# Kernel tuning notes

Hardware: AMD Instinct MI355X
Metric: run time of the kernel (lower is better)

## Reference

```python
import jax, jax.numpy as jnp
import numpy as np
from math import sqrt

D_MODEL = 512
HEADS = 8
D_K = D_MODEL // HEADS
DIM_FFN = 2048
EPS = 1e-6


def setup_inputs() -> dict:
    key = jax.random.key(0)
    ks = jax.random.split(key, 16)
    b, s = 2, 256
    inp = {
        "x": jax.random.normal(ks[0], (b, s, D_MODEL), dtype=jnp.float32),
        "connection_bias_k": jax.random.normal(ks[1], (b, s, s, D_MODEL), dtype=jnp.float32) * 0.02,
        "connection_bias_v": jax.random.normal(ks[2], (b, s, s, D_MODEL), dtype=jnp.float32) * 0.02,
        "mask": jnp.zeros((b, s), dtype=jnp.int32),
        "Wq": jax.random.normal(ks[3], (D_MODEL, D_MODEL), dtype=jnp.float32) / sqrt(D_MODEL),
        "bq": jnp.zeros((D_MODEL,), dtype=jnp.float32),
        "Wk": jax.random.normal(ks[4], (D_MODEL, D_MODEL), dtype=jnp.float32) / sqrt(D_MODEL),
        "bk": jnp.zeros((D_MODEL,), dtype=jnp.float32),
        "Wv": jax.random.normal(ks[5], (D_MODEL, D_MODEL), dtype=jnp.float32) / sqrt(D_MODEL),
        "bv": jnp.zeros((D_MODEL,), dtype=jnp.float32),
        "Wo": jax.random.normal(ks[6], (D_MODEL, D_MODEL), dtype=jnp.float32) / sqrt(D_MODEL),
        "bo": jnp.zeros((D_MODEL,), dtype=jnp.float32),
        "alpha1": jnp.ones((D_MODEL,), dtype=jnp.float32),
        "beta1": jnp.zeros((D_MODEL,), dtype=jnp.float32),
        "alpha2": jnp.ones((D_MODEL,), dtype=jnp.float32),
        "beta2": jnp.zeros((D_MODEL,), dtype=jnp.float32),
        "W1": jax.random.normal(ks[7], (DIM_FFN, D_MODEL), dtype=jnp.float32) / sqrt(D_MODEL),
        "b1": jnp.zeros((DIM_FFN,), dtype=jnp.float32),
        "W2": jax.random.normal(ks[8], (D_MODEL, DIM_FFN), dtype=jnp.float32) / sqrt(DIM_FFN),
        "b2": jnp.zeros((D_MODEL,), dtype=jnp.float32),
    }
    return inp


def _norm(x, alpha, beta):
    # torch .std() is unbiased (ddof=1); note std is added to eps OUTSIDE variance
    mu = jnp.mean(x, axis=-1, keepdims=True)
    sd = jnp.std(x, axis=-1, ddof=1, keepdims=True)
    return alpha * (x - mu) / (sd + EPS) + beta


def reference(x, connection_bias_k, connection_bias_v, mask,
              Wq, bq, Wk, bk, Wv, bv, Wo, bo,
              alpha1, beta1, alpha2, beta2, W1, b1, W2, b2):
    b, s, _ = x.shape
    h, dk = HEADS, D_K

    x2 = _norm(x, alpha1, beta1)
    # projections -> [b, h, s, dk]
    q = (x2 @ Wq.T + bq).reshape(b, s, h, dk).transpose(0, 2, 1, 3)
    k = (x2 @ Wk.T + bk).reshape(b, s, h, dk).transpose(0, 2, 1, 3)
    v = (x2 @ Wv.T + bv).reshape(b, s, h, dk).transpose(0, 2, 1, 3)

    # biases reshaped to (b, s1, s2, h, dk); biased_k[b,h,i,j] = k[b,h,j] + bias[b,j,i,h]
    bk_r = connection_bias_k.reshape(b, s, s, h, dk)
    bv_r = connection_bias_v.reshape(b, s, s, h, dk)

    # scores[b,h,i,j] = q_i . (k_j + bias_k[b,j,i,h]) / sqrt(dk)
    scores = (jnp.einsum('bhid,bhjd->bhij', q, k)
              + jnp.einsum('bhid,bjihd->bhij', q, bk_r)) / sqrt(dk)

    # mask [b,s] -> [b,1,s,1], broadcast over heads and key dim (matches torch)
    m = mask[:, None, :, None]
    scores = jnp.where(m == 1, -1e9, scores)
    attn = jax.nn.softmax(scores, axis=-1)

    # out[b,h,i,d] = sum_j attn[b,h,i,j] * (v[b,h,j] + bias_v[b,j,i,h])
    out = (jnp.einsum('bhij,bhjd->bhid', attn, v)
           + jnp.einsum('bhij,bjihd->bhid', attn, bv_r))
    concat = out.transpose(0, 2, 1, 3).reshape(b, s, D_MODEL)
    attn_out = concat @ Wo.T + bo

    x = x + attn_out
    x2 = _norm(x, alpha2, beta2)
    ff = jax.nn.relu(x2 @ W1.T + b1) @ W2.T + b2
    return x + ff
```

## Files before the change

### kernel.cpp

```cpp
#include <hip/hip_runtime.h>
#include <math.h>

#define D_MODEL 512
#define NHEADS 8
#define DK 64
#define DFFN 2048

__global__ __launch_bounds__(256) void ln_kernel(
    const float* __restrict__ x, const float* __restrict__ alpha,
    const float* __restrict__ beta, float* __restrict__ y) {
  int row = blockIdx.x;
  int t = threadIdx.x;
  const float* xr = x + (size_t)row * D_MODEL;
  float2 v = ((const float2*)xr)[t];
  __shared__ float rs[256], rq[256];
  rs[t] = v.x + v.y;
  rq[t] = v.x * v.x + v.y * v.y;
  __syncthreads();
  for (int o = 128; o > 0; o >>= 1) {
    if (t < o) { rs[t] += rs[t + o]; rq[t] += rq[t + o]; }
    __syncthreads();
  }
  float mu = rs[0] * (1.0f / D_MODEL);
  float var = (rq[0] - (float)D_MODEL * mu * mu) * (1.0f / (D_MODEL - 1));
  float inv = 1.0f / (sqrtf(fmaxf(var, 0.0f)) + 1e-6f);
  float2 a2 = ((const float2*)alpha)[t];
  float2 b2 = ((const float2*)beta)[t];
  float2 o2;
  o2.x = a2.x * (v.x - mu) * inv + b2.x;
  o2.y = a2.y * (v.y - mu) * inv + b2.y;
  ((float2*)(y + (size_t)row * D_MODEL))[t] = o2;
}

template <int RELU>
__global__ __launch_bounds__(256) void gemm_nt(
    const float* __restrict__ A, const float* __restrict__ B,
    const float* __restrict__ bias, const float* __restrict__ res,
    float* __restrict__ C, int M, int N, int K) {
  __shared__ float As[16][65];
  __shared__ float Bs[16][65];
  int t = threadIdx.x;
  int tx = t & 15, ty = t >> 4;
  int ldRow = t >> 2;
  int ldCol = (t & 3) << 2;
  const float* Ap = A + (size_t)(blockIdx.y * 64 + ldRow) * K + ldCol;
  const float* Bp = B + (size_t)(blockIdx.x * 64 + ldRow) * K + ldCol;
  float acc[4][4] = {};
  for (int k0 = 0; k0 < K; k0 += 16) {
    float4 a4 = *(const float4*)(Ap + k0);
    float4 b4 = *(const float4*)(Bp + k0);
    As[ldCol + 0][ldRow] = a4.x; As[ldCol + 1][ldRow] = a4.y;
    As[ldCol + 2][ldRow] = a4.z; As[ldCol + 3][ldRow] = a4.w;
    Bs[ldCol + 0][ldRow] = b4.x; Bs[ldCol + 1][ldRow] = b4.y;
    Bs[ldCol + 2][ldRow] = b4.z; Bs[ldCol + 3][ldRow] = b4.w;
    __syncthreads();
#pragma unroll
    for (int kk = 0; kk < 16; ++kk) {
      float a[4], b[4];
#pragma unroll
      for (int i = 0; i < 4; ++i) a[i] = As[kk][ty * 4 + i];
#pragma unroll
      for (int j = 0; j < 4; ++j) b[j] = Bs[kk][tx * 4 + j];
#pragma unroll
      for (int i = 0; i < 4; ++i)
#pragma unroll
        for (int j = 0; j < 4; ++j) acc[i][j] += a[i] * b[j];
    }
    __syncthreads();
  }
  int row0 = blockIdx.y * 64 + ty * 4;
  int col0 = blockIdx.x * 64 + tx * 4;
#pragma unroll
  for (int i = 0; i < 4; ++i) {
#pragma unroll
    for (int j = 0; j < 4; ++j) {
      float v = acc[i][j] + bias[col0 + j];
      if (res) v += res[(size_t)(row0 + i) * N + col0 + j];
      if (RELU) v = fmaxf(v, 0.0f);
      C[(size_t)(row0 + i) * N + col0 + j] = v;
    }
  }
}

struct Triple { const float* B; const float* bias; float* C; };
struct Triple3 { Triple t[3]; };

__global__ __launch_bounds__(256) void gemm_qkv(
    const float* __restrict__ A, Triple3 p3, int M, int N, int K) {
  Triple tr = p3.t[blockIdx.z];
  const float* __restrict__ B = tr.B;
  __shared__ float As[16][65];
  __shared__ float Bs[16][65];
  int t = threadIdx.x;
  int tx = t & 15, ty = t >> 4;
  int ldRow = t >> 2;
  int ldCol = (t & 3) << 2;
  const float* Ap = A + (size_t)(blockIdx.y * 64 + ldRow) * K + ldCol;
  const float* Bp = B + (size_t)(blockIdx.x * 64 + ldRow) * K + ldCol;
  float acc[4][4] = {};
  for (int k0 = 0; k0 < K; k0 += 16) {
    float4 a4 = *(const float4*)(Ap + k0);
    float4 b4 = *(const float4*)(Bp + k0);
    As[ldCol + 0][ldRow] = a4.x; As[ldCol + 1][ldRow] = a4.y;
    As[ldCol + 2][ldRow] = a4.z; As[ldCol + 3][ldRow] = a4.w;
    Bs[ldCol + 0][ldRow] = b4.x; Bs[ldCol + 1][ldRow] = b4.y;
    Bs[ldCol + 2][ldRow] = b4.z; Bs[ldCol + 3][ldRow] = b4.w;
    __syncthreads();
#pragma unroll
    for (int kk = 0; kk < 16; ++kk) {
      float a[4], b[4];
#pragma unroll
      for (int i = 0; i < 4; ++i) a[i] = As[kk][ty * 4 + i];
#pragma unroll
      for (int j = 0; j < 4; ++j) b[j] = Bs[kk][tx * 4 + j];
#pragma unroll
      for (int i = 0; i < 4; ++i)
#pragma unroll
        for (int j = 0; j < 4; ++j) acc[i][j] += a[i] * b[j];
    }
    __syncthreads();
  }
  int row0 = blockIdx.y * 64 + ty * 4;
  int col0 = blockIdx.x * 64 + tx * 4;
#pragma unroll
  for (int i = 0; i < 4; ++i) {
#pragma unroll
    for (int j = 0; j < 4; ++j) {
      tr.C[(size_t)(row0 + i) * N + col0 + j] = acc[i][j] + tr.bias[col0 + j];
    }
  }
}

__global__ __launch_bounds__(256) void gemm_nt_splitk(
    const float* __restrict__ A, const float* __restrict__ B,
    float* __restrict__ P, int M, int N, int K, int KC) {
  __shared__ float As[16][65];
  __shared__ float Bs[16][65];
  int t = threadIdx.x;
  int tx = t & 15, ty = t >> 4;
  int ldRow = t >> 2;
  int ldCol = (t & 3) << 2;
  int kbase = blockIdx.z * KC;
  const float* Ap = A + (size_t)(blockIdx.y * 64 + ldRow) * K + ldCol + kbase;
  const float* Bp = B + (size_t)(blockIdx.x * 64 + ldRow) * K + ldCol + kbase;
  float acc[4][4] = {};
  for (int k0 = 0; k0 < KC; k0 += 16) {
    float4 a4 = *(const float4*)(Ap + k0);
    float4 b4 = *(const float4*)(Bp + k0);
    As[ldCol + 0][ldRow] = a4.x; As[ldCol + 1][ldRow] = a4.y;
    As[ldCol + 2][ldRow] = a4.z; As[ldCol + 3][ldRow] = a4.w;
    Bs[ldCol + 0][ldRow] = b4.x; Bs[ldCol + 1][ldRow] = b4.y;
    Bs[ldCol + 2][ldRow] = b4.z; Bs[ldCol + 3][ldRow] = b4.w;
    __syncthreads();
#pragma unroll
    for (int kk = 0; kk < 16; ++kk) {
      float a[4], b[4];
#pragma unroll
      for (int i = 0; i < 4; ++i) a[i] = As[kk][ty * 4 + i];
#pragma unroll
      for (int j = 0; j < 4; ++j) b[j] = Bs[kk][tx * 4 + j];
#pragma unroll
      for (int i = 0; i < 4; ++i)
#pragma unroll
        for (int j = 0; j < 4; ++j) acc[i][j] += a[i] * b[j];
    }
    __syncthreads();
  }
  int row0 = blockIdx.y * 64 + ty * 4;
  int col0 = blockIdx.x * 64 + tx * 4;
  float* Pz = P + (size_t)blockIdx.z * M * N;
#pragma unroll
  for (int i = 0; i < 4; ++i)
#pragma unroll
    for (int j = 0; j < 4; ++j)
      Pz[(size_t)(row0 + i) * N + col0 + j] = acc[i][j];
}

__global__ __launch_bounds__(256) void splitk_reduce(
    const float* __restrict__ P, const float* __restrict__ bias,
    const float* __restrict__ res, float* __restrict__ C,
    int MN, int N, int Z) {
  int idx = blockIdx.x * 256 + threadIdx.x;
  if (idx >= MN) return;
  float v = bias[idx % N] + res[idx];
  for (int z = 0; z < Z; ++z) v += P[(size_t)z * MN + idx];
  C[idx] = v;
}

__global__ __launch_bounds__(256) void attn_kernel(
    const float* __restrict__ q, const float* __restrict__ k,
    const float* __restrict__ v, const float* __restrict__ cbk,
    const float* __restrict__ cbv, const int* __restrict__ mask,
    float* __restrict__ concat, int s) {
  int i = blockIdx.x % s;
  int h = (blockIdx.x / s) % NHEADS;
  int b = blockIdx.x / (s * NHEADS);
  int t = threadIdx.x;

  __shared__ __align__(16) float qs[DK];
  __shared__ float p[256];
  __shared__ float red[256];
  __shared__ float outp[4][DK];

  size_t qbase = ((size_t)(b * s + i)) * D_MODEL + h * DK;
  if (t < DK) qs[t] = q[qbase + t];
  __syncthreads();

  int lane16 = t & 15;
  int jg = t >> 4;
  float4 q4 = ((const float4*)qs)[lane16];
  for (int jt = 0; jt < s; jt += 16) {
    int j = jt + jg;
    size_t kb = ((size_t)(b * s + j)) * D_MODEL + h * DK + lane16 * 4;
    float4 k4 = *(const float4*)(k + kb);
    size_t bb = (((size_t)(b * s + j)) * s + i) * D_MODEL + h * DK + lane16 * 4;
    float4 b4 = *(const float4*)(cbk + bb);
    float part = q4.x * (k4.x + b4.x) + q4.y * (k4.y + b4.y) +
                 q4.z * (k4.z + b4.z) + q4.w * (k4.w + b4.w);
    part += __shfl_xor(part, 1);
    part += __shfl_xor(part, 2);
    part += __shfl_xor(part, 4);
    part += __shfl_xor(part, 8);
    if (lane16 == 0) p[j] = part * 0.125f;
  }
  __syncthreads();

  float sc = p[t];
  if (mask[b * s + i] == 1) sc = -1e9f;
  red[t] = sc;
  __syncthreads();
  for (int o = 128; o > 0; o >>= 1) {
    if (t < o) red[t] = fmaxf(red[t], red[t + o]);
    __syncthreads();
  }
  float mx = red[0];
  __syncthreads();
  float e = expf(sc - mx);
  p[t] = e;
  red[t] = e;
  __syncthreads();
  for (int o = 128; o > 0; o >>= 1) {
    if (t < o) red[t] += red[t + o];
    __syncthreads();
  }
  float inv = 1.0f / red[0];

  int d = t & 63;
  int c = t >> 6;
  float acc = 0.0f;
  int chunk = s >> 2;
  for (int jj = 0; jj < chunk; ++jj) {
    int j = c * chunk + jj;
    size_t vb = ((size_t)(b * s + j)) * D_MODEL + h * DK + d;
    size_t bb = (((size_t)(b * s + j)) * s + i) * D_MODEL + h * DK + d;
    acc += p[j] * (v[vb] + cbv[bb]);
  }
  outp[c][d] = acc;
  __syncthreads();
  if (t < DK) {
    float o = (outp[0][t] + outp[1][t] + outp[2][t] + outp[3][t]) * inv;
    concat[((size_t)(b * s + i)) * D_MODEL + h * DK + t] = o;
  }
}

extern "C" void kernel_launch(void* const* d_in, const int* in_sizes, int n_in,
                              void* d_out, int out_size, void* d_ws, size_t ws_size,
                              hipStream_t stream) {
  const float* x      = (const float*)d_in[0];
  const float* cbk    = (const float*)d_in[1];
  const float* cbv    = (const float*)d_in[2];
  const int*   mask   = (const int*)d_in[3];
  const float* Wq     = (const float*)d_in[4];
  const float* bq     = (const float*)d_in[5];
  const float* Wk     = (const float*)d_in[6];
  const float* bk     = (const float*)d_in[7];
  const float* Wv     = (const float*)d_in[8];
  const float* bv     = (const float*)d_in[9];
  const float* Wo     = (const float*)d_in[10];
  const float* bo     = (const float*)d_in[11];
  const float* alpha1 = (const float*)d_in[12];
  const float* beta1  = (const float*)d_in[13];
  const float* alpha2 = (const float*)d_in[14];
  const float* beta2  = (const float*)d_in[15];
  const float* W1     = (const float*)d_in[16];
  const float* b1     = (const float*)d_in[17];
  const float* W2     = (const float*)d_in[18];
  const float* b2     = (const float*)d_in[19];

  int bs = in_sizes[0] / D_MODEL;
  int s  = in_sizes[1] / in_sizes[0];
  int b  = bs / s;

  float* ws = (float*)d_ws;
  float* x2      = ws;
  float* qb      = x2 + (size_t)bs * D_MODEL;
  float* kb      = qb + (size_t)bs * D_MODEL;
  float* vb      = kb + (size_t)bs * D_MODEL;
  float* concat  = vb + (size_t)bs * D_MODEL;
  float* xres    = concat + (size_t)bs * D_MODEL;
  float* x2b     = xres + (size_t)bs * D_MODEL;
  float* f1      = x2b + (size_t)bs * D_MODEL;
  float* partial = f1 + (size_t)bs * DFFN;

  ln_kernel<<<bs, 256, 0, stream>>>(x, alpha1, beta1, x2);

  Triple3 p3;
  p3.t[0] = {Wq, bq, qb};
  p3.t[1] = {Wk, bk, kb};
  p3.t[2] = {Wv, bv, vb};
  gemm_qkv<<<dim3(D_MODEL / 64, bs / 64, 3), 256, 0, stream>>>(x2, p3, bs, D_MODEL, D_MODEL);

  attn_kernel<<<b * NHEADS * s, 256, 0, stream>>>(qb, kb, vb, cbk, cbv, mask, concat, s);

  gemm_nt<0><<<dim3(D_MODEL / 64, bs / 64), 256, 0, stream>>>(
      concat, Wo, bo, x, xres, bs, D_MODEL, D_MODEL);

  ln_kernel<<<bs, 256, 0, stream>>>(xres, alpha2, beta2, x2b);

  gemm_nt<1><<<dim3(DFFN / 64, bs / 64), 256, 0, stream>>>(
      x2b, W1, b1, nullptr, f1, bs, DFFN, D_MODEL);

  gemm_nt_splitk<<<dim3(D_MODEL / 64, bs / 64, 4), 256, 0, stream>>>(
      f1, W2, partial, bs, D_MODEL, DFFN, DFFN / 4);
  splitk_reduce<<<(bs * D_MODEL + 255) / 256, 256, 0, stream>>>(
      partial, b2, xres, (float*)d_out, bs * D_MODEL, D_MODEL, 4);
}
```

Baseline: 727.8 us.

## Switch GEMMs to bf16 MFMA and restructure attention per token across heads

```diff
diff --git a/kernel.cpp b/kernel.cpp
--- a/kernel.cpp
+++ b/kernel.cpp
@@ -6,9 +6,12 @@
 #define DK 64
 #define DFFN 2048
 
+typedef __attribute__((ext_vector_type(8))) __bf16 bf16x8;
+typedef __attribute__((ext_vector_type(4))) float floatx4;
+
 __global__ __launch_bounds__(256) void ln_kernel(
     const float* __restrict__ x, const float* __restrict__ alpha,
-    const float* __restrict__ beta, float* __restrict__ y) {
+    const float* __restrict__ beta, __bf16* __restrict__ y) {
   int row = blockIdx.x;
   int t = threadIdx.x;
   const float* xr = x + (size_t)row * D_MODEL;
@@ -26,241 +29,178 @@
   float inv = 1.0f / (sqrtf(fmaxf(var, 0.0f)) + 1e-6f);
   float2 a2 = ((const float2*)alpha)[t];
   float2 b2 = ((const float2*)beta)[t];
-  float2 o2;
-  o2.x = a2.x * (v.x - mu) * inv + b2.x;
-  o2.y = a2.y * (v.y - mu) * inv + b2.y;
-  ((float2*)(y + (size_t)row * D_MODEL))[t] = o2;
-}
-
-template <int RELU>
-__global__ __launch_bounds__(256) void gemm_nt(
-    const float* __restrict__ A, const float* __restrict__ B,
+  union { __bf16 h2[2]; unsigned int u; } pk;
+  pk.h2[0] = (__bf16)(a2.x * (v.x - mu) * inv + b2.x);
+  pk.h2[1] = (__bf16)(a2.y * (v.y - mu) * inv + b2.y);
+  *(unsigned int*)(y + (size_t)row * D_MODEL + 2 * t) = pk.u;
+}
+
+struct Seg { const float* src; __bf16* dst; int n4; };
+struct Segs6 { Seg s[6]; };
+__global__ __launch_bounds__(256) void cast6(Segs6 cs) {
+  Seg sg = cs.s[blockIdx.y];
+  int stride = gridDim.x * 256;
+  for (int idx = blockIdx.x * 256 + threadIdx.x; idx < sg.n4; idx += stride) {
+    float4 f = ((const float4*)sg.src)[idx];
+    union { __bf16 h[4]; uint2 u; } pk;
+    pk.h[0] = (__bf16)f.x; pk.h[1] = (__bf16)f.y;
+    pk.h[2] = (__bf16)f.z; pk.h[3] = (__bf16)f.w;
+    ((uint2*)sg.dst)[idx] = pk.u;
+  }
+}
+
+__global__ __launch_bounds__(256) void pack_bias(
+    const float* __restrict__ bq, const float* __restrict__ bk,
+    const float* __restrict__ bv, float* __restrict__ dst) {
+  int idx = blockIdx.x * 256 + threadIdx.x;
+  if (idx >= 3 * D_MODEL) return;
+  float v = idx < 512 ? bq[idx] : (idx < 1024 ? bk[idx - 512] : bv[idx - 1024]);
+  dst[idx] = v;
+}
+
+template <int RELU, int OUT_BF16>
+__global__ __launch_bounds__(64) void wave_gemm(
+    const __bf16* __restrict__ A, int lda, const __bf16* __restrict__ B, int ldb,
     const float* __restrict__ bias, const float* __restrict__ res,
-    float* __restrict__ C, int M, int N, int K) {
-  __shared__ float As[16][65];
-  __shared__ float Bs[16][65];
+    void* __restrict__ Cv, int N, int K) {
+  int lane = threadIdx.x;
+  int r16 = lane & 15;
+  int ko = (lane >> 4) * 8;
+  int m0 = blockIdx.y * 32, n0 = blockIdx.x * 32;
+  const __bf16* A0 = A + (size_t)(m0 + r16) * lda + ko;
+  const __bf16* A1 = A0 + (size_t)16 * lda;
+  const __bf16* B0 = B + (size_t)(n0 + r16) * ldb + ko;
+  const __bf16* B1 = B0 + (size_t)16 * ldb;
+  floatx4 acc00 = {0.f, 0.f, 0.f, 0.f};
+  floatx4 acc01 = acc00, acc10 = acc00, acc11 = acc00;
+#pragma unroll 4
+  for (int k0 = 0; k0 < K; k0 += 32) {
+    bf16x8 a0 = *(const bf16x8*)(A0 + k0);
+    bf16x8 a1 = *(const bf16x8*)(A1 + k0);
+    bf16x8 b0 = *(const bf16x8*)(B0 + k0);
+    bf16x8 b1 = *(const bf16x8*)(B1 + k0);
+    acc00 = __builtin_amdgcn_mfma_f32_16x16x32_bf16(a0, b0, acc00, 0, 0, 0);
+    acc01 = __builtin_amdgcn_mfma_f32_16x16x32_bf16(a0, b1, acc01, 0, 0, 0);
+    acc10 = __builtin_amdgcn_mfma_f32_16x16x32_bf16(a1, b0, acc10, 0, 0, 0);
+    acc11 = __builtin_amdgcn_mfma_f32_16x16x32_bf16(a1, b1, acc11, 0, 0, 0);
+  }
+  int col = lane & 15, rb = (lane >> 4) * 4;
+  floatx4 accs[2][2] = {{acc00, acc01}, {acc10, acc11}};
+#pragma unroll
+  for (int i = 0; i < 2; ++i) {
+#pragma unroll
+    for (int j = 0; j < 2; ++j) {
+#pragma unroll
+      for (int r = 0; r < 4; ++r) {
+        int row = m0 + i * 16 + rb + r;
+        int cc = n0 + j * 16 + col;
+        float v = accs[i][j][r] + bias[cc];
+        if (res) v += res[(size_t)row * N + cc];
+        if (RELU) v = fmaxf(v, 0.0f);
+        if (OUT_BF16)
+          ((__bf16*)Cv)[(size_t)row * N + cc] = (__bf16)v;
+        else
+          ((float*)Cv)[(size_t)row * N + cc] = v;
+      }
+    }
+  }
+}
+
+__global__ __launch_bounds__(256) void attn_kernel(
+    const float* __restrict__ qkv, int ldq,
+    const float* __restrict__ cbk, const float* __restrict__ cbv,
+    const int* __restrict__ mask, __bf16* __restrict__ concat, int s) {
+  int i = blockIdx.x % s;
+  int b = blockIdx.x / s;
   int t = threadIdx.x;
-  int tx = t & 15, ty = t >> 4;
-  int ldRow = t >> 2;
-  int ldCol = (t & 3) << 2;
-  const float* Ap = A + (size_t)(blockIdx.y * 64 + ldRow) * K + ldCol;
-  const float* Bp = B + (size_t)(blockIdx.x * 64 + ldRow) * K + ldCol;
-  float acc[4][4] = {};
-  for (int k0 = 0; k0 < K; k0 += 16) {
-    float4 a4 = *(const float4*)(Ap + k0);
-    float4 b4 = *(const float4*)(Bp + k0);
-    As[ldCol + 0][ldRow] = a4.x; As[ldCol + 1][ldRow] = a4.y;
-    As[ldCol + 2][ldRow] = a4.z; As[ldCol + 3][ldRow] = a4.w;
-    Bs[ldCol + 0][ldRow] = b4.x; Bs[ldCol + 1][ldRow] = b4.y;
-    Bs[ldCol + 2][ldRow] = b4.z; Bs[ldCol + 3][ldRow] = b4.w;
-    __syncthreads();
-#pragma unroll
-    for (int kk = 0; kk < 16; ++kk) {
-      float a[4], b[4];
-#pragma unroll
-      for (int i = 0; i < 4; ++i) a[i] = As[kk][ty * 4 + i];
-#pragma unroll
-      for (int j = 0; j < 4; ++j) b[j] = Bs[kk][tx * 4 + j];
-#pragma unroll
-      for (int i = 0; i < 4; ++i)
-#pragma unroll
-        for (int j = 0; j < 4; ++j) acc[i][j] += a[i] * b[j];
+  int w = t >> 6;
+  int lane = t & 63;
+  int h = lane >> 3;
+
+  __shared__ float sc[NHEADS][257];
+  __shared__ float sums[NHEADS];
+  __shared__ float part[4][D_MODEL];
+
+  size_t tok_i = (size_t)(b * s + i);
+  const float* qp = qkv + tok_i * ldq + lane * 8;
+  float4 q0 = *(const float4*)(qp);
+  float4 q1 = *(const float4*)(qp + 4);
+
+  for (int jj = 0; jj < 64; ++jj) {
+    int j = w * 64 + jj;
+    size_t tok_j = (size_t)(b * s + j);
+    const float* kp = qkv + tok_j * ldq + 512 + lane * 8;
+    const float* cp = cbk + (tok_j * s + i) * D_MODEL + lane * 8;
+    float4 k0 = *(const float4*)(kp);
+    float4 k1 = *(const float4*)(kp + 4);
+    float4 c0 = *(const float4*)(cp);
+    float4 c1 = *(const float4*)(cp + 4);
+    float d = q0.x * (k0.x + c0.x) + q0.y * (k0.y + c0.y) +
+              q0.z * (k0.z + c0.z) + q0.w * (k0.w + c0.w) +
+              q1.x * (k1.x + c1.x) + q1.y * (k1.y + c1.y) +
+              q1.z * (k1.z + c1.z) + q1.w * (k1.w + c1.w);
+    d += __shfl_xor(d, 1);
+    d += __shfl_xor(d, 2);
+    d += __shfl_xor(d, 4);
+    if ((lane & 7) == 0) sc[h][j] = d * 0.125f;
+  }
+  __syncthreads();
+
+  {
+    int hh = 2 * w + (lane >> 5);
+    int l32 = lane & 31;
+    bool masked = (mask[b * s + i] == 1);
+    float vals[8];
+    float mx = -1e30f;
+#pragma unroll
+    for (int kk = 0; kk < 8; ++kk) {
+      float xv = sc[hh][l32 + kk * 32];
+      if (masked) xv = -1e9f;
+      vals[kk] = xv;
+      mx = fmaxf(mx, xv);
     }
-    __syncthreads();
-  }
-  int row0 = blockIdx.y * 64 + ty * 4;
-  int col0 = blockIdx.x * 64 + tx * 4;
-#pragma unroll
-  for (int i = 0; i < 4; ++i) {
-#pragma unroll
-    for (int j = 0; j < 4; ++j) {
-      float v = acc[i][j] + bias[col0 + j];
-      if (res) v += res[(size_t)(row0 + i) * N + col0 + j];
-      if (RELU) v = fmaxf(v, 0.0f);
-      C[(size_t)(row0 + i) * N + col0 + j] = v;
+    for (int m = 1; m < 32; m <<= 1) mx = fmaxf(mx, __shfl_xor(mx, m, 32));
+    float ls = 0.f;
+#pragma unroll
+    for (int kk = 0; kk < 8; ++kk) {
+      float e = expf(vals[kk] - mx);
+      sc[hh][l32 + kk * 32] = e;
+      ls += e;
     }
-  }
-}
-
-struct Triple { const float* B; const float* bias; float* C; };
-struct Triple3 { Triple t[3]; };
-
-__global__ __launch_bounds__(256) void gemm_qkv(
-    const float* __restrict__ A, Triple3 p3, int M, int N, int K) {
-  Triple tr = p3.t[blockIdx.z];
-  const float* __restrict__ B = tr.B;
-  __shared__ float As[16][65];
-  __shared__ float Bs[16][65];
-  int t = threadIdx.x;
-  int tx = t & 15, ty = t >> 4;
-  int ldRow = t >> 2;
-  int ldCol = (t & 3) << 2;
-  const float* Ap = A + (size_t)(blockIdx.y * 64 + ldRow) * K + ldCol;
-  const float* Bp = B + (size_t)(blockIdx.x * 64 + ldRow) * K + ldCol;
-  float acc[4][4] = {};
-  for (int k0 = 0; k0 < K; k0 += 16) {
-    float4 a4 = *(const float4*)(Ap + k0);
-    float4 b4 = *(const float4*)(Bp + k0);
-    As[ldCol + 0][ldRow] = a4.x; As[ldCol + 1][ldRow] = a4.y;
-    As[ldCol + 2][ldRow] = a4.z; As[ldCol + 3][ldRow] = a4.w;
-    Bs[ldCol + 0][ldRow] = b4.x; Bs[ldCol + 1][ldRow] = b4.y;
-    Bs[ldCol + 2][ldRow] = b4.z; Bs[ldCol + 3][ldRow] = b4.w;
-    __syncthreads();
-#pragma unroll
-    for (int kk = 0; kk < 16; ++kk) {
-      float a[4], b[4];
-#pragma unroll
-      for (int i = 0; i < 4; ++i) a[i] = As[kk][ty * 4 + i];
-#pragma unroll
-      for (int j = 0; j < 4; ++j) b[j] = Bs[kk][tx * 4 + j];
-#pragma unroll
-      for (int i = 0; i < 4; ++i)
-#pragma unroll
-        for (int j = 0; j < 4; ++j) acc[i][j] += a[i] * b[j];
-    }
-    __syncthreads();
-  }
-  int row0 = blockIdx.y * 64 + ty * 4;
-  int col0 = blockIdx.x * 64 + tx * 4;
-#pragma unroll
-  for (int i = 0; i < 4; ++i) {
-#pragma unroll
-    for (int j = 0; j < 4; ++j) {
-      tr.C[(size_t)(row0 + i) * N + col0 + j] = acc[i][j] + tr.bias[col0 + j];
-    }
-  }
-}
-
-__global__ __launch_bounds__(256) void gemm_nt_splitk(
-    const float* __restrict__ A, const float* __restrict__ B,
-    float* __restrict__ P, int M, int N, int K, int KC) {
-  __shared__ float As[16][65];
-  __shared__ float Bs[16][65];
-  int t = threadIdx.x;
-  int tx = t & 15, ty = t >> 4;
-  int ldRow = t >> 2;
-  int ldCol = (t & 3) << 2;
-  int kbase = blockIdx.z * KC;
-  const float* Ap = A + (size_t)(blockIdx.y * 64 + ldRow) * K + ldCol + kbase;
-  const float* Bp = B + (size_t)(blockIdx.x * 64 + ldRow) * K + ldCol + kbase;
-  float acc[4][4] = {};
-  for (int k0 = 0; k0 < KC; k0 += 16) {
-    float4 a4 = *(const float4*)(Ap + k0);
-    float4 b4 = *(const float4*)(Bp + k0);
-    As[ldCol + 0][ldRow] = a4.x; As[ldCol + 1][ldRow] = a4.y;
-    As[ldCol + 2][ldRow] = a4.z; As[ldCol + 3][ldRow] = a4.w;
-    Bs[ldCol + 0][ldRow] = b4.x; Bs[ldCol + 1][ldRow] = b4.y;
-    Bs[ldCol + 2][ldRow] = b4.z; Bs[ldCol + 3][ldRow] = b4.w;
-    __syncthreads();
-#pragma unroll
-    for (int kk = 0; kk < 16; ++kk) {
-      float a[4], b[4];
-#pragma unroll
-      for (int i = 0; i < 4; ++i) a[i] = As[kk][ty * 4 + i];
-#pragma unroll
-      for (int j = 0; j < 4; ++j) b[j] = Bs[kk][tx * 4 + j];
-#pragma unroll
-      for (int i = 0; i < 4; ++i)
-#pragma unroll
-        for (int j = 0; j < 4; ++j) acc[i][j] += a[i] * b[j];
-    }
-    __syncthreads();
-  }
-  int row0 = blockIdx.y * 64 + ty * 4;
-  int col0 = blockIdx.x * 64 + tx * 4;
-  float* Pz = P + (size_t)blockIdx.z * M * N;
-#pragma unroll
-  for (int i = 0; i < 4; ++i)
-#pragma unroll
-    for (int j = 0; j < 4; ++j)
-      Pz[(size_t)(row0 + i) * N + col0 + j] = acc[i][j];
-}
-
-__global__ __launch_bounds__(256) void splitk_reduce(
-    const float* __restrict__ P, const float* __restrict__ bias,
-    const float* __restrict__ res, float* __restrict__ C,
-    int MN, int N, int Z) {
-  int idx = blockIdx.x * 256 + threadIdx.x;
-  if (idx >= MN) return;
-  float v = bias[idx % N] + res[idx];
-  for (int z = 0; z < Z; ++z) v += P[(size_t)z * MN + idx];
-  C[idx] = v;
-}
-
-__global__ __launch_bounds__(256) void attn_kernel(
-    const float* __restrict__ q, const float* __restrict__ k,
-    const float* __restrict__ v, const float* __restrict__ cbk,
-    const float* __restrict__ cbv, const int* __restrict__ mask,
-    float* __restrict__ concat, int s) {
-  int i = blockIdx.x % s;
-  int h = (blockIdx.x / s) % NHEADS;
-  int b = blockIdx.x / (s * NHEADS);
-  int t = threadIdx.x;
-
-  __shared__ __align__(16) float qs[DK];
-  __shared__ float p[256];
-  __shared__ float red[256];
-  __shared__ float outp[4][DK];
-
-  size_t qbase = ((size_t)(b * s + i)) * D_MODEL + h * DK;
-  if (t < DK) qs[t] = q[qbase + t];
-  __syncthreads();
-
-  int lane16 = t & 15;
-  int jg = t >> 4;
-  float4 q4 = ((const float4*)qs)[lane16];
-  for (int jt = 0; jt < s; jt += 16) {
-    int j = jt + jg;
-    size_t kb = ((size_t)(b * s + j)) * D_MODEL + h * DK + lane16 * 4;
-    float4 k4 = *(const float4*)(k + kb);
-    size_t bb = (((size_t)(b * s + j)) * s + i) * D_MODEL + h * DK + lane16 * 4;
-    float4 b4 = *(const float4*)(cbk + bb);
-    float part = q4.x * (k4.x + b4.x) + q4.y * (k4.y + b4.y) +
-                 q4.z * (k4.z + b4.z) + q4.w * (k4.w + b4.w);
-    part += __shfl_xor(part, 1);
-    part += __shfl_xor(part, 2);
-    part += __shfl_xor(part, 4);
-    part += __shfl_xor(part, 8);
-    if (lane16 == 0) p[j] = part * 0.125f;
-  }
-  __syncthreads();
-
-  float sc = p[t];
-  if (mask[b * s + i] == 1) sc = -1e9f;
-  red[t] = sc;
-  __syncthreads();
-  for (int o = 128; o > 0; o >>= 1) {
-    if (t < o) red[t] = fmaxf(red[t], red[t + o]);
-    __syncthreads();
-  }
-  float mx = red[0];
-  __syncthreads();
-  float e = expf(sc - mx);
-  p[t] = e;
-  red[t] = e;
-  __syncthreads();
-  for (int o = 128; o > 0; o >>= 1) {
-    if (t < o) red[t] += red[t + o];
-    __syncthreads();
-  }
-  float inv = 1.0f / red[0];
-
-  int d = t & 63;
-  int c = t >> 6;
-  float acc = 0.0f;
-  int chunk = s >> 2;
-  for (int jj = 0; jj < chunk; ++jj) {
-    int j = c * chunk + jj;
-    size_t vb = ((size_t)(b * s + j)) * D_MODEL + h * DK + d;
-    size_t bb = (((size_t)(b * s + j)) * s + i) * D_MODEL + h * DK + d;
-    acc += p[j] * (v[vb] + cbv[bb]);
-  }
-  outp[c][d] = acc;
-  __syncthreads();
-  if (t < DK) {
-    float o = (outp[0][t] + outp[1][t] + outp[2][t] + outp[3][t]) * inv;
-    concat[((size_t)(b * s + i)) * D_MODEL + h * DK + t] = o;
-  }
+    for (int m = 1; m < 32; m <<= 1) ls += __shfl_xor(ls, m, 32);
+    if (l32 == 0) sums[hh] = ls;
+  }
+  __syncthreads();
+
+  float4 a0 = {0.f, 0.f, 0.f, 0.f};
+  float4 a1 = {0.f, 0.f, 0.f, 0.f};
+  for (int jj = 0; jj < 64; ++jj) {
+    int j = w * 64 + jj;
+    size_t tok_j = (size_t)(b * s + j);
+    const float* vp = qkv + tok_j * ldq + 1024 + lane * 8;
+    const float* cp = cbv + (tok_j * s + i) * D_MODEL + lane * 8;
+    float4 v0 = *(const float4*)(vp);
+    float4 v1 = *(const float4*)(vp + 4);
+    float4 c0 = *(const float4*)(cp);
+    float4 c1 = *(const float4*)(cp + 4);
+    float pj = sc[h][j];
+    a0.x += pj * (v0.x + c0.x); a0.y += pj * (v0.y + c0.y);
+    a0.z += pj * (v0.z + c0.z); a0.w += pj * (v0.w + c0.w);
+    a1.x += pj * (v1.x + c1.x); a1.y += pj * (v1.y + c1.y);
+    a1.z += pj * (v1.z + c1.z); a1.w += pj * (v1.w + c1.w);
+  }
+  *(float4*)&part[w][lane * 8] = a0;
+  *(float4*)&part[w][lane * 8 + 4] = a1;
+  __syncthreads();
+
+  int d0 = t * 2;
+  float inv = 1.0f / sums[d0 >> 6];
+  float o0 = (part[0][d0] + part[1][d0] + part[2][d0] + part[3][d0]) * inv;
+  float o1 = (part[0][d0 + 1] + part[1][d0 + 1] + part[2][d0 + 1] + part[3][d0 + 1]) * inv;
+  union { __bf16 h2[2]; unsigned int u; } pk;
+  pk.h2[0] = (__bf16)o0;
+  pk.h2[1] = (__bf16)o1;
+  *(unsigned int*)(concat + tok_i * D_MODEL + d0) = pk.u;
 }
 
 extern "C" void kernel_launch(void* const* d_in, const int* in_sizes, int n_in,
@@ -289,39 +229,50 @@
 
   int bs = in_sizes[0] / D_MODEL;
   int s  = in_sizes[1] / in_sizes[0];
-  int b  = bs / s;
-
-  float* ws = (float*)d_ws;
-  float* x2      = ws;
-  float* qb      = x2 + (size_t)bs * D_MODEL;
-  float* kb      = qb + (size_t)bs * D_MODEL;
-  float* vb      = kb + (size_t)bs * D_MODEL;
-  float* concat  = vb + (size_t)bs * D_MODEL;
-  float* xres    = concat + (size_t)bs * D_MODEL;
-  float* x2b     = xres + (size_t)bs * D_MODEL;
-  float* f1      = x2b + (size_t)bs * D_MODEL;
-  float* partial = f1 + (size_t)bs * DFFN;
+
+  char* wp = (char*)d_ws;
+  auto carve = [&](size_t bytes) {
+    char* p = wp;
+    wp += (bytes + 255) & ~(size_t)255;
+    return p;
+  };
+  __bf16* x2    = (__bf16*)carve((size_t)bs * D_MODEL * 2);
+  __bf16* wqkv  = (__bf16*)carve((size_t)3 * D_MODEL * D_MODEL * 2);
+  __bf16* wo_b  = (__bf16*)carve((size_t)D_MODEL * D_MODEL * 2);
+  __bf16* w1_b  = (__bf16*)carve((size_t)DFFN * D_MODEL * 2);
+  __bf16* w2_b  = (__bf16*)carve((size_t)D_MODEL * DFFN * 2);
+  float*  bqkv  = (float*)carve((size_t)3 * D_MODEL * 4);
+  float*  qkv   = (float*)carve((size_t)bs * 3 * D_MODEL * 4);
+  __bf16* conc  = (__bf16*)carve((size_t)bs * D_MODEL * 2);
+  float*  xres  = (float*)carve((size_t)bs * D_MODEL * 4);
+  __bf16* x2b   = (__bf16*)carve((size_t)bs * D_MODEL * 2);
+  __bf16* f1    = (__bf16*)carve((size_t)bs * DFFN * 2);
+
+  Segs6 cs;
+  cs.s[0] = {Wq, wqkv,                 D_MODEL * D_MODEL / 4};
+  cs.s[1] = {Wk, wqkv + D_MODEL * D_MODEL,     D_MODEL * D_MODEL / 4};
+  cs.s[2] = {Wv, wqkv + 2 * D_MODEL * D_MODEL, D_MODEL * D_MODEL / 4};
+  cs.s[3] = {Wo, wo_b, D_MODEL * D_MODEL / 4};
+  cs.s[4] = {W1, w1_b, DFFN * D_MODEL / 4};
+  cs.s[5] = {W2, w2_b, D_MODEL * DFFN / 4};
+  cast6<<<dim3(256, 6), 256, 0, stream>>>(cs);
+  pack_bias<<<6, 256, 0, stream>>>(bq, bk, bv, bqkv);
 
   ln_kernel<<<bs, 256, 0, stream>>>(x, alpha1, beta1, x2);
 
-  Triple3 p3;
-  p3.t[0] = {Wq, bq, qb};
-  p3.t[1] = {Wk, bk, kb};
-  p3.t[2] = {Wv, bv, vb};
-  gemm_qkv<<<dim3(D_MODEL / 64, bs / 64, 3), 256, 0, stream>>>(x2, p3, bs, D_MODEL, D_MODEL);
-
-  attn_kernel<<<b * NHEADS * s, 256, 0, stream>>>(qb, kb, vb, cbk, cbv, mask, concat, s);
-
-  gemm_nt<0><<<dim3(D_MODEL / 64, bs / 64), 256, 0, stream>>>(
-      concat, Wo, bo, x, xres, bs, D_MODEL, D_MODEL);
+  wave_gemm<0, 0><<<dim3(3 * D_MODEL / 32, bs / 32), 64, 0, stream>>>(
+      x2, D_MODEL, wqkv, D_MODEL, bqkv, nullptr, qkv, 3 * D_MODEL, D_MODEL);
+
+  attn_kernel<<<bs, 256, 0, stream>>>(qkv, 3 * D_MODEL, cbk, cbv, mask, conc, s);
+
+  wave_gemm<0, 0><<<dim3(D_MODEL / 32, bs / 32), 64, 0, stream>>>(
+      conc, D_MODEL, wo_b, D_MODEL, bo, x, xres, D_MODEL, D_MODEL);
 
   ln_kernel<<<bs, 256, 0, stream>>>(xres, alpha2, beta2, x2b);
 
-  gemm_nt<1><<<dim3(DFFN / 64, bs / 64), 256, 0, stream>>>(
-      x2b, W1, b1, nullptr, f1, bs, DFFN, D_MODEL);
-
-  gemm_nt_splitk<<<dim3(D_MODEL / 64, bs / 64, 4), 256, 0, stream>>>(
-      f1, W2, partial, bs, D_MODEL, DFFN, DFFN / 4);
-  splitk_reduce<<<(bs * D_MODEL + 255) / 256, 256, 0, stream>>>(
-      partial, b2, xres, (float*)d_out, bs * D_MODEL, D_MODEL, 4);
-}
+  wave_gemm<1, 1><<<dim3(DFFN / 32, bs / 32), 64, 0, stream>>>(
+      x2b, D_MODEL, w1_b, D_MODEL, b1, nullptr, f1, DFFN, D_MODEL);
+
+  wave_gemm<0, 0><<<dim3(D_MODEL / 32, bs / 32), 64, 0, stream>>>(
+      f1, DFFN, w2_b, DFFN, b2, xres, d_out, D_MODEL, DFFN);
+}
```

Result: faster. 609.6 us (-16.2%).
